# Performance work log

Measured on AMD Instinct MI355X. Metric: run time of the kernel, lower is better.

## Reference

```python
import jax, jax.numpy as jnp
import numpy as np

IMAGE_TOKEN_INDEX = -200
B, N, D = 2, 768, 2048          # batch, seq, llm_size
CLIP = 1024                      # clip hidden size
NUM_HEADS = 8
HEAD_DIM = CLIP // NUM_HEADS
NUM_LAYER, LAYER_RATE = 24, 4
LAYER_IDX = np.asarray(NUM_LAYER - np.arange(0, NUM_LAYER + 1, LAYER_RATE))  # [24,20,16,12,8,4,0]
J = len(LAYER_IDX)               # 7 selected layers
L = NUM_LAYER + 1                # 25 stacked layers in all_features
IMG, PATCH = 336, 14
HP = IMG // PATCH                # 24 patches per side; patch_ratio == 1
HW = HP * HP                     # 576 vision tokens
SL = HP * (HP + 1) + 1           # 601 = H*(W+1)+1 ragged slice length
SCALE = CLIP ** (-0.5)
LN_EPS = 1e-5
COS_EPS = 1e-8


def setup_inputs() -> dict:
    key = jax.random.key(0)
    ks = jax.random.split(key, 10)
    input_ids = jax.random.randint(ks[0], (B, N), 0, 32000)
    pos = jnp.array([37, 111])  # image-token positions; pos + SL <= N
    input_ids = input_ids.at[jnp.arange(B), pos].set(IMAGE_TOKEN_INDEX)
    rgb = jax.random.normal(ks[1], (B, 3, IMG, IMG), dtype=jnp.float32)
    mask = jnp.ones((B, 1, IMG, IMG), dtype=jnp.float32)  # last channel: all-ones mask
    images = jnp.concatenate([rgb, mask], axis=1)
    all_features = jax.random.normal(ks[2], (B, N, L, D), dtype=jnp.float32)
    patch_hw = jnp.full((B, 2), HP, dtype=jnp.int32)
    s = 0.02
    return {
        'input_ids': input_ids,
        'images': images,
        'all_features': all_features,
        'patch_hw': patch_hw,
        'norm_gamma': jnp.ones((J, D), dtype=jnp.float32),
        'norm_beta': jnp.zeros((J, D), dtype=jnp.float32),
        'norm_w': jax.random.normal(ks[3], (J, CLIP, D), dtype=jnp.float32) * s,
        'input_w': jax.random.normal(ks[4], (CLIP, D), dtype=jnp.float32) * s,
        'input_b': jnp.zeros((CLIP,), dtype=jnp.float32),
        'output_w': jax.random.normal(ks[5], (CLIP, CLIP), dtype=jnp.float32) * s,
        'output_b': jnp.zeros((CLIP,), dtype=jnp.float32),
        'clip_w': jax.random.normal(ks[6], (CLIP, 3 * PATCH * PATCH), dtype=jnp.float32) * s,
        'clip_b': jnp.zeros((CLIP,), dtype=jnp.float32),
    }


def reference(input_ids, images, all_features, patch_hw,
              norm_gamma, norm_beta, norm_w,
              input_w, input_b, output_w, output_b, clip_w, clip_b):
    # clip_layer modeled as a frozen 14x14 patch-embed linear -> [B, HW, CLIP]
    patches = images[:, :3].reshape(B, 3, HP, PATCH, HP, PATCH)
    patches = patches.transpose(0, 2, 4, 1, 3, 5).reshape(B, HW, 3 * PATCH * PATCH)
    clip_feats = patches @ clip_w.T + clip_b  # [B, HW, CLIP]
    # mask channel is all ones -> pooled clip_2d_mask keeps every patch
    lidx = jnp.asarray(LAYER_IDX)

    def per_sample(ids, feats, cf):
        # ragged slice at the image token (data-dependent start, fixed length)
        idx = jnp.argmax(ids == IMAGE_TOKEN_INDEX)
        f = jax.lax.dynamic_slice_in_dim(feats, idx, SL, axis=0)[1:]      # [600, L, D]
        # [L,D,H,W+1] drop-last-col in torch == row-major split here
        f = f.reshape(HP, HP + 1, L, D)[:, :HP].reshape(HW, L, D)          # [576, L, D]
        # per-layer LayerNorm + no-bias Linear on 7 selected layers
        xj = f[:, lidx]                                                    # [HW, J, D]
        mu = xj.mean(-1, keepdims=True)
        var = ((xj - mu) ** 2).mean(-1, keepdims=True)
        xn = (xj - mu) / jnp.sqrt(var + LN_EPS) * norm_gamma + norm_beta
        vis = jnp.einsum('njd,jcd->njc', xn, norm_w)                       # [HW, J, CLIP]
        inp = f[:, -1] @ input_w.T + input_b                               # [HW, CLIP]
        # single-query multi-head cross attention over the J-1 kv layers
        q = vis[:, 0].reshape(HW, NUM_HEADS, HEAD_DIM)                     # [HW, h, d]
        kv = vis[:, 1:].reshape(HW, J - 1, NUM_HEADS, HEAD_DIM).transpose(0, 2, 1, 3)  # [HW, h, J-1, d]
        attn = jax.nn.softmax((q[:, :, None, :] * SCALE * kv).sum(-1), axis=-1)        # [HW, h, J-1]
        fuse = (attn[..., None] * kv).sum(-2).reshape(HW, CLIP)
        out = inp + fuse @ output_w.T + output_b                           # [HW, CLIP]
        denom = jnp.maximum(jnp.linalg.norm(out, axis=-1) * jnp.linalg.norm(cf, axis=-1), COS_EPS)
        cos = (out * cf).sum(-1) / denom
        return 1.0 - cos.mean()

    losses = jax.vmap(per_sample)(input_ids, all_features, clip_feats)
    return losses.mean()  # mse_loss / count_image with count_image == B
```

## Files before the change

### kernel.cpp

```cpp
#include <hip/hip_runtime.h>

#define HW_   576
#define BHW   1152
#define DD    2048
#define CLIPC 1024
#define NSEQ  768
#define LL    25
#define KPAD  640

#define ASCALE 8.0f
#define BSCALE 32.0f
#define INV_AB (1.0f/256.0f)

typedef __bf16 bf16x8 __attribute__((ext_vector_type(8)));
typedef float  f32x4  __attribute__((ext_vector_type(4)));
typedef int    i32x8  __attribute__((ext_vector_type(8)));
typedef unsigned short u16;
typedef unsigned char  u8;

__device__ __forceinline__ float bf2f(u16 u){
  union { unsigned int i; float f; } v; v.i = ((unsigned int)u) << 16; return v.f;
}
__device__ __forceinline__ u16 f2bf(float f){
  union { float f; unsigned int i; } v; v.f = f;
  unsigned int u = v.i;
  return (u16)((u + 0x7fffu + ((u >> 16) & 1u)) >> 16);
}
__device__ __forceinline__ unsigned int pk2bf(float a, float b){
  return ((unsigned int)f2bf(a)) | (((unsigned int)f2bf(b)) << 16);
}
__device__ __forceinline__ unsigned int pk4_fp8(float a, float b, float c, float d){
  int v = 0;
  v = __builtin_amdgcn_cvt_pk_fp8_f32(a, b, v, false);
  v = __builtin_amdgcn_cvt_pk_fp8_f32(c, d, v, true);
  return (unsigned int)v;
}

__device__ __forceinline__ void gld_lds16(const void* g, void* l){
  __builtin_amdgcn_global_load_lds((__attribute__((address_space(1))) void*)g,
                                   (__attribute__((address_space(3))) void*)l,
                                   16, 0, 0);
}

__global__ void prep_k(const float* __restrict__ norm_w, const float* __restrict__ input_w,
                       const float* __restrict__ output_w, const float* __restrict__ clip_w,
                       const float* __restrict__ images, const float* __restrict__ feats,
                       const int* __restrict__ ids,
                       const float* __restrict__ gamma, const float* __restrict__ beta,
                       u8* __restrict__ B8, u16* __restrict__ inpw, u16* __restrict__ outw,
                       u16* __restrict__ clipw, u16* __restrict__ patch,
                       u8* __restrict__ A8, u16* __restrict__ A7,
                       float* __restrict__ rowacc, unsigned int* __restrict__ done){
  const int blk = blockIdx.x, tid = threadIdx.x;
  if (blk < 7168){
    long idx = (long)blk*2048 + tid*8;
    float4 v0 = *(const float4*)(norm_w + idx);
    float4 v1 = *(const float4*)(norm_w + idx + 4);
    uint2 o;
    o.x = pk4_fp8(v0.x*BSCALE, v0.y*BSCALE, v0.z*BSCALE, v0.w*BSCALE);
    o.y = pk4_fp8(v1.x*BSCALE, v1.y*BSCALE, v1.z*BSCALE, v1.w*BSCALE);
    *(uint2*)(B8 + idx) = o;
    return;
  }
  if (blk < 8704){
    const bool isInp = (blk < 8192);
    long idx = (long)(blk - (isInp ? 7168 : 8192))*2048 + tid*8;
    const float* s = isInp ? (input_w + idx) : (output_w + idx);
    float4 v0 = *(const float4*)s;
    float4 v1 = *(const float4*)(s + 4);
    uint4 o = { pk2bf(v0.x,v0.y), pk2bf(v0.z,v0.w), pk2bf(v1.x,v1.y), pk2bf(v1.z,v1.w) };
    *(uint4*)((isInp ? inpw : outw) + idx) = o;
    return;
  }
  if (blk < 9728){
    const int c = blk - 8704;
    for (int k = tid; k < KPAD; k += 256)
      clipw[c*KPAD + k] = (k < 588) ? f2bf(clip_w[c*588 + k]) : (u16)0;
    if (blk == 8704){
      for (int i = tid; i < BHW*4; i += 256) rowacc[i] = 0.f;
      if (tid == 0) *done = 0u;
    }
    return;
  }
  if (blk < 10880){
    const int r = blk - 9728;
    const int b = r / HW_, n = r % HW_;
    const int hi = n / 24, wi = n % 24;
    for (int p = tid; p < KPAD; p += 256){
      float v = 0.f;
      if (p < 588){
        int c3 = p / 196, rem = p - c3*196;
        int ph = rem / 14, pw = rem - ph*14;
        v = images[(((long)b*4 + c3)*336 + hi*14 + ph)*336 + wi*14 + pw];
      }
      patch[(long)r*KPAD + p] = f2bf(v);
    }
    return;
  }
  const int q = blk - 10880;
  const int r = q >> 3, g = q & 7;
  const int b = r / HW_, n = r % HW_;
  const int hi = n / 24, wi = n % 24;
  __shared__ int ridx[4];
  __shared__ float rs[4], rq[4];
  {
    int best = 0x7fffffff;
    for (int i = tid; i < NSEQ; i += 256)
      if (ids[b*NSEQ + i] == -200 && i < best) best = i;
    for (int off = 32; off; off >>= 1){ int o = __shfl_xor(best, off); best = min(best, o); }
    if ((tid & 63) == 0) ridx[tid >> 6] = best;
    __syncthreads();
  }
  const int tok = min(min(ridx[0],ridx[1]),min(ridx[2],ridx[3])) + 1 + hi*25 + wi;
  const int layer = (g < 7) ? (24 - g*4) : 24;
  const float* src = feats + (((long)(b*NSEQ + tok))*LL + layer)*DD + tid*8;
  float4 a = *(const float4*)src;
  float4 c = *(const float4*)(src + 4);
  if (g == 7){
    uint4 o = { pk2bf(a.x,a.y), pk2bf(a.z,a.w), pk2bf(c.x,c.y), pk2bf(c.z,c.w) };
    *(uint4*)(A7 + (long)r*DD + tid*8) = o;
    return;
  }
  float s  = a.x+a.y+a.z+a.w + c.x+c.y+c.z+c.w;
  float qq = a.x*a.x+a.y*a.y+a.z*a.z+a.w*a.w + c.x*c.x+c.y*c.y+c.z*c.z+c.w*c.w;
  for (int off = 32; off; off >>= 1){ s += __shfl_xor(s, off); qq += __shfl_xor(qq, off); }
  const int wave = tid >> 6, lane = tid & 63;
  if (lane == 0){ rs[wave] = s; rq[wave] = qq; }
  __syncthreads();
  const float ts = rs[0]+rs[1]+rs[2]+rs[3];
  const float tq = rq[0]+rq[1]+rq[2]+rq[3];
  const float mu   = ts * (1.f/2048.f);
  const float var  = tq * (1.f/2048.f) - mu*mu;
  const float rstd = rsqrtf(var + 1e-5f);
  const float4 g0 = *(const float4*)(gamma + g*DD + tid*8);
  const float4 g1 = *(const float4*)(gamma + g*DD + tid*8 + 4);
  const float4 b0 = *(const float4*)(beta  + g*DD + tid*8);
  const float4 b1 = *(const float4*)(beta  + g*DD + tid*8 + 4);
  uint2 o;
  o.x = pk4_fp8(((a.x-mu)*rstd*g0.x + b0.x)*ASCALE, ((a.y-mu)*rstd*g0.y + b0.y)*ASCALE,
                ((a.z-mu)*rstd*g0.z + b0.z)*ASCALE, ((a.w-mu)*rstd*g0.w + b0.w)*ASCALE);
  o.y = pk4_fp8(((c.x-mu)*rstd*g1.x + b1.x)*ASCALE, ((c.y-mu)*rstd*g1.y + b1.y)*ASCALE,
                ((c.z-mu)*rstd*g1.z + b1.z)*ASCALE, ((c.w-mu)*rstd*g1.w + b1.w)*ASCALE);
  *(uint2*)(A8 + ((long)g*BHW + r)*DD + tid*8) = o;
}

__global__ __launch_bounds__(256, 3)
void gemm9_k(const u8* __restrict__ A8, const u8* __restrict__ B8,
             u16* __restrict__ C_all, const u16* __restrict__ A7,
             const u16* __restrict__ inpw, const u16* __restrict__ patch,
             const u16* __restrict__ clipw, float* __restrict__ cf,
             const float* __restrict__ input_b, const float* __restrict__ clip_b){
  __shared__ alignas(16) u8 smem[32768];
  const int z = blockIdx.z;
  const int bm = blockIdx.x*128, bn = blockIdx.y*128;
  const int tid = threadIdx.x, wave = tid >> 6, lane = tid & 63;
  const int l15 = lane & 15, quad = lane >> 4;
  const int wr = (wave >> 1)*64, wc = (wave & 1)*64;
  f32x4 acc[4][4] = {};
  const int laneRow   = lane >> 3;
  const int laneChunk = (lane & 7) ^ laneRow;

  if (z < 7){
    u8* As = smem;
    u8* Bs = smem + 16384;
    const u8* Az = A8 + (long)z*BHW*DD;
    const u8* Bz = B8 + (long)z*CLIPC*DD;
    const u8* gA = Az + (long)(bm + wave*32 + laneRow)*DD + laneChunk*16;
    const u8* gB = Bz + (long)(bn + wave*32 + laneRow)*DD + laneChunk*16;
    u8* lA = &As[wave*32*128];
    u8* lB = &Bs[wave*32*128];
    const long rs8 = 8L*DD;
    for (int k0 = 0; k0 < DD; k0 += 128){
#pragma unroll
      for (int t = 0; t < 4; t++) gld_lds16(gA + k0 + t*rs8, lA + t*1024);
#pragma unroll
      for (int t = 0; t < 4; t++) gld_lds16(gB + k0 + t*rs8, lB + t*1024);
      __syncthreads();
      i32x8 af[4], bg[4];
      const int sw = l15 & 7;
#pragma unroll
      for (int i = 0; i < 4; i++){
        const u8* rp = &As[(wr + i*16 + l15)*128];
        uint4 lo = *(const uint4*)(rp + (((quad*2 + 0) ^ sw)*16));
        uint4 hi = *(const uint4*)(rp + (((quad*2 + 1) ^ sw)*16));
        af[i] = (i32x8){(int)lo.x,(int)lo.y,(int)lo.z,(int)lo.w,
                        (int)hi.x,(int)hi.y,(int)hi.z,(int)hi.w};
      }
#pragma unroll
      for (int j = 0; j < 4; j++){
        const u8* rp = &Bs[(wc + j*16 + l15)*128];
        uint4 lo = *(const uint4*)(rp + (((quad*2 + 0) ^ sw)*16));
        uint4 hi = *(const uint4*)(rp + (((quad*2 + 1) ^ sw)*16));
        bg[j] = (i32x8){(int)lo.x,(int)lo.y,(int)lo.z,(int)lo.w,
                        (int)hi.x,(int)hi.y,(int)hi.z,(int)hi.w};
      }
#pragma unroll
      for (int i = 0; i < 4; i++)
#pragma unroll
        for (int j = 0; j < 4; j++)
          acc[i][j] = __builtin_amdgcn_mfma_scale_f32_16x16x128_f8f6f4(
              af[i], bg[j], acc[i][j], 0, 0, 0, 0x7F7F7F7F, 0, 0x7F7F7F7F);
      __syncthreads();
    }
    u16* C = C_all + (long)z*BHW*CLIPC;
#pragma unroll
    for (int i = 0; i < 4; i++)
#pragma unroll
      for (int j = 0; j < 4; j++)
#pragma unroll
        for (int rr = 0; rr < 4; rr++){
          const int row = bm + wr + i*16 + quad*4 + rr;
          const int col = bn + wc + j*16 + l15;
          C[(long)row*CLIPC + col] = f2bf(acc[i][j][rr] * INV_AB);
        }
  } else {
    u16* As = (u16*)smem;
    u16* Bs = (u16*)(smem + 16384);
    const u16* Az = (z == 7) ? A7   : patch;
    const u16* Bz = (z == 7) ? inpw : clipw;
    const int K  = (z == 7) ? DD : KPAD;
    const int laneCol = laneChunk * 8;
    const u16* gA = Az + (long)(bm + wave*32 + laneRow)*K + laneCol;
    const u16* gB = Bz + (long)(bn + wave*32 + laneRow)*K + laneCol;
    u16* lA = &As[wave*2048];
    u16* lB = &Bs[wave*2048];
    const long rs8 = (long)8 * K;
    for (int k0 = 0; k0 < K; k0 += 64){
#pragma unroll
      for (int t = 0; t < 4; t++) gld_lds16(gA + k0 + t*rs8, lA + t*512);
#pragma unroll
      for (int t = 0; t < 4; t++) gld_lds16(gB + k0 + t*rs8, lB + t*512);
      __syncthreads();
#pragma unroll
      for (int s = 0; s < 2; s++){
        bf16x8 af[4], bg[4];
#pragma unroll
        for (int i = 0; i < 4; i++)
          af[i] = *(const bf16x8*)&As[(wr + i*16 + l15)*64 + (((s*4 + quad) ^ (l15 & 7))*8)];
#pragma unroll
        for (int j = 0; j < 4; j++)
          bg[j] = *(const bf16x8*)&Bs[(wc + j*16 + l15)*64 + (((s*4 + quad) ^ (l15 & 7))*8)];
#pragma unroll
        for (int i = 0; i < 4; i++)
#pragma unroll
          for (int j = 0; j < 4; j++)
            acc[i][j] = __builtin_amdgcn_mfma_f32_16x16x32_bf16(af[i], bg[j], acc[i][j], 0, 0, 0);
      }
      __syncthreads();
    }
    if (z == 7){
      u16* C = C_all + 7L*BHW*CLIPC;
#pragma unroll
      for (int i = 0; i < 4; i++)
#pragma unroll
        for (int j = 0; j < 4; j++)
#pragma unroll
          for (int rr = 0; rr < 4; rr++){
            const int row = bm + wr + i*16 + quad*4 + rr;
            const int col = bn + wc + j*16 + l15;
            C[(long)row*CLIPC + col] = f2bf(acc[i][j][rr] + input_b[col]);
          }
    } else {
#pragma unroll
      for (int i = 0; i < 4; i++)
#pragma unroll
        for (int j = 0; j < 4; j++)
#pragma unroll
          for (int rr = 0; rr < 4; rr++){
            const int row = bm + wr + i*16 + quad*4 + rr;
            const int col = bn + wc + j*16 + l15;
            cf[(long)row*CLIPC + col] = acc[i][j][rr] + clip_b[col];
          }
    }
  }
}

__global__ void attn_k(const u16* __restrict__ C_all, u16* __restrict__ fuse){
  const int r = blockIdx.x;
  const int h = (blockIdx.y << 2) | (threadIdx.x >> 6);
  const int lane = threadIdx.x & 63;
  const long slot = (long)BHW * CLIPC;
  const long rb = (long)r * CLIPC;
  const int c0 = h*128 + lane, c1 = c0 + 64;
  const float q0 = bf2f(C_all[rb + c0]), q1 = bf2f(C_all[rb + c1]);
  float k0v[6], k1v[6], dt[6];
#pragma unroll
  for (int t = 0; t < 6; t++){
    const u16* base = C_all + (long)(t+1)*slot + rb;
    k0v[t] = bf2f(base[c0]); k1v[t] = bf2f(base[c1]);
    dt[t] = q0*k0v[t] + q1*k1v[t];
  }
#pragma unroll
  for (int t = 0; t < 6; t++)
    for (int off = 32; off; off >>= 1) dt[t] += __shfl_xor(dt[t], off);
  float l[6], e[6];
#pragma unroll
  for (int t = 0; t < 6; t++) l[t] = dt[t] * 0.03125f;
  float m = l[0];
#pragma unroll
  for (int t = 1; t < 6; t++) m = fmaxf(m, l[t]);
  float ssum = 0.f;
#pragma unroll
  for (int t = 0; t < 6; t++){ e[t] = __expf(l[t] - m); ssum += e[t]; }
  const float inv = 1.f / ssum;
  float f0 = 0.f, f1 = 0.f;
#pragma unroll
  for (int t = 0; t < 6; t++){ const float a = e[t]*inv; f0 += a*k0v[t]; f1 += a*k1v[t]; }
  fuse[rb + c0] = f2bf(f0);
  fuse[rb + c1] = f2bf(f1);
}

__global__ __launch_bounds__(256, 3)
void gemm_out_k(const u16* __restrict__ fuse, const u16* __restrict__ outw,
                const u16* __restrict__ inp, const float* __restrict__ output_b,
                const float* __restrict__ cf, float* __restrict__ rowacc,
                unsigned int* __restrict__ done, float* __restrict__ out){
  __shared__ alignas(16) u8 smem[32768];
  u16* As = (u16*)smem;
  u16* Bs = (u16*)(smem + 16384);
  const int bm = blockIdx.x*128, bn = blockIdx.y*128;
  const int tid = threadIdx.x, wave = tid >> 6, lane = tid & 63;
  const int l15 = lane & 15, quad = lane >> 4;
  const int wr = (wave >> 1)*64, wc = (wave & 1)*64;
  f32x4 acc[4][4] = {};
  {
    const int laneRow = lane >> 3;
    const int laneCol = (((lane & 7) ^ laneRow) * 8);
    const u16* gA = fuse + (long)(bm + wave*32 + laneRow)*CLIPC + laneCol;
    const u16* gB = outw + (long)(bn + wave*32 + laneRow)*CLIPC + laneCol;
    u16* lA = &As[wave*2048];
    u16* lB = &Bs[wave*2048];
    const long rs8 = 8L*CLIPC;
    for (int k0 = 0; k0 < CLIPC; k0 += 64){
#pragma unroll
      for (int t = 0; t < 4; t++) gld_lds16(gA + k0 + t*rs8, lA + t*512);
#pragma unroll
      for (int t = 0; t < 4; t++) gld_lds16(gB + k0 + t*rs8, lB + t*512);
      __syncthreads();
#pragma unroll
      for (int s = 0; s < 2; s++){
        bf16x8 af[4], bg[4];
#pragma unroll
        for (int i = 0; i < 4; i++)
          af[i] = *(const bf16x8*)&As[(wr + i*16 + l15)*64 + (((s*4 + quad) ^ (l15 & 7))*8)];
#pragma unroll
        for (int j = 0; j < 4; j++)
          bg[j] = *(const bf16x8*)&Bs[(wc + j*16 + l15)*64 + (((s*4 + quad) ^ (l15 & 7))*8)];
#pragma unroll
        for (int i = 0; i < 4; i++)
#pragma unroll
          for (int j = 0; j < 4; j++)
            acc[i][j] = __builtin_amdgcn_mfma_f32_16x16x32_bf16(af[i], bg[j], acc[i][j], 0, 0, 0);
      }
      __syncthreads();
    }
  }
#pragma unroll
  for (int i = 0; i < 4; i++)
#pragma unroll
    for (int rr = 0; rr < 4; rr++){
      const int row = bm + wr + i*16 + quad*4 + rr;
      float soc = 0.f, soo = 0.f, scc = 0.f;
#pragma unroll
      for (int j = 0; j < 4; j++){
        const int col = bn + wc + j*16 + l15;
        const long p = (long)row*CLIPC + col;
        const float o = acc[i][j][rr] + output_b[col] + bf2f(inp[p]);
        const float c = cf[p];
        soc += o*c; soo += o*o; scc += c*c;
      }
#pragma unroll
      for (int off = 1; off < 16; off <<= 1){
        soc += __shfl_xor(soc, off); soo += __shfl_xor(soo, off); scc += __shfl_xor(scc, off);
      }
      if (l15 == 0){
        atomicAdd(&rowacc[row*4 + 0], soc);
        atomicAdd(&rowacc[row*4 + 1], soo);
        atomicAdd(&rowacc[row*4 + 2], scc);
      }
    }
  __threadfence();
  __shared__ unsigned int amLast;
  if (tid == 0) amLast = (atomicAdd(done, 1u) == 71u) ? 1u : 0u;
  __syncthreads();
  if (!amLast) return;
  float s = 0.f;
  for (int r = tid; r < BHW; r += 256){
    const float soc = __hip_atomic_load(&rowacc[r*4+0], __ATOMIC_RELAXED, __HIP_MEMORY_SCOPE_AGENT);
    const float soo = __hip_atomic_load(&rowacc[r*4+1], __ATOMIC_RELAXED, __HIP_MEMORY_SCOPE_AGENT);
    const float scc = __hip_atomic_load(&rowacc[r*4+2], __ATOMIC_RELAXED, __HIP_MEMORY_SCOPE_AGENT);
    s += soc / fmaxf(sqrtf(soo*scc), 1e-8f);
  }
  for (int off = 32; off; off >>= 1) s += __shfl_xor(s, off);
  __shared__ float fr[4];
  if ((tid & 63) == 0) fr[tid >> 6] = s;
  __syncthreads();
  if (tid == 0) out[0] = 1.f - (fr[0]+fr[1]+fr[2]+fr[3]) * (1.f/(float)BHW);
}

extern "C" void kernel_launch(void* const* d_in, const int* in_sizes, int n_in,
                              void* d_out, int out_size, void* d_ws, size_t ws_size,
                              hipStream_t stream){
  const int*   input_ids = (const int*)  d_in[0];
  const float* images    = (const float*)d_in[1];
  const float* all_feats = (const float*)d_in[2];
  const float* norm_gamma = (const float*)d_in[4];
  const float* norm_beta  = (const float*)d_in[5];
  const float* norm_w     = (const float*)d_in[6];
  const float* input_w    = (const float*)d_in[7];
  const float* input_b    = (const float*)d_in[8];
  const float* output_w   = (const float*)d_in[9];
  const float* output_b   = (const float*)d_in[10];
  const float* clip_w     = (const float*)d_in[11];
  const float* clip_b     = (const float*)d_in[12];
  float* out = (float*)d_out;

  char* w = (char*)d_ws;
  unsigned int* done = (unsigned int*)w;
  size_t off = 256;
  u8*  A8    = (u8*) (w + off); off += 7L*BHW*DD;
  u16* A7    = (u16*)(w + off); off += (long)BHW*DD*2;
  u8*  B8    = (u8*) (w + off); off += 7L*CLIPC*DD;
  u16* inpw  = (u16*)(w + off); off += (long)CLIPC*DD*2;
  u16* outw  = (u16*)(w + off); off += (long)CLIPC*CLIPC*2;
  u16* clipw = (u16*)(w + off); off += (long)CLIPC*KPAD*2;
  u16* patch = (u16*)(w + off); off += (long)BHW*KPAD*2;
  u16* C_all = (u16*)(w + off); off += 8L*BHW*CLIPC*2;
  u16* fuse  = (u16*)(w + off); off += (long)BHW*CLIPC*2;
  float* cf     = (float*)(w + off); off += (long)BHW*CLIPC*4;
  float* rowacc = (float*)(w + off); off += (long)BHW*4*4;

  prep_k<<<20096, 256, 0, stream>>>(norm_w, input_w, output_w, clip_w, images, all_feats,
                                    input_ids, norm_gamma, norm_beta,
                                    B8, inpw, outw, clipw, patch, A8, A7, rowacc, done);
  gemm9_k<<<dim3(9, 8, 9), 256, 0, stream>>>(A8, B8, C_all, A7, inpw, patch, clipw, cf,
                                             input_b, clip_b);
  attn_k<<<dim3(1152, 2), 256, 0, stream>>>(C_all, fuse);
  gemm_out_k<<<dim3(9, 8), 256, 0, stream>>>(fuse, outw, C_all + 7L*BHW*CLIPC,
                                             output_b, cf, rowacc, done, out);
}
```

Before: 531.9 us.

## Interleave GEMM problem blocks in flat grid and double-buffer output GEMM loads

The batched GEMM kernel now runs on a flattened 1D grid. Its first 576 blocks interleave the eight big GEMMs (z = f & 7), and the patch/clip GEMM tiles come last, so blocks working on the same tile position but different layers run together and the cheap K=640 work fills the tail. Separately, the output GEMM double-buffers its LDS tiles (64 KB) and prefetches the next K-slice while computing the current one. That overlap costs occupancy, since launch bounds drop to 2 blocks per CU. The output GEMM has only 72 blocks, so the lower occupancy limit hardly matters there.

```diff
diff --git a/kernel.cpp b/kernel.cpp
--- a/kernel.cpp
+++ b/kernel.cpp
@@ -151,8 +151,10 @@
              const u16* __restrict__ clipw, float* __restrict__ cf,
              const float* __restrict__ input_b, const float* __restrict__ clip_b){
   __shared__ alignas(16) u8 smem[32768];
-  const int z = blockIdx.z;
-  const int bm = blockIdx.x*128, bn = blockIdx.y*128;
+  const int f = blockIdx.x;
+  int z, t;
+  if (f < 576){ z = f & 7; t = f >> 3; } else { z = 8; t = f - 576; }
+  const int bm = (t % 9)*128, bn = (t / 9)*128;
   const int tid = threadIdx.x, wave = tid >> 6, lane = tid & 63;
   const int l15 = lane & 15, quad = lane >> 4;
   const int wr = (wave >> 1)*64, wc = (wave & 1)*64;
@@ -172,9 +174,9 @@
     const long rs8 = 8L*DD;
     for (int k0 = 0; k0 < DD; k0 += 128){
 #pragma unroll
-      for (int t = 0; t < 4; t++) gld_lds16(gA + k0 + t*rs8, lA + t*1024);
-#pragma unroll
-      for (int t = 0; t < 4; t++) gld_lds16(gB + k0 + t*rs8, lB + t*1024);
+      for (int t2 = 0; t2 < 4; t2++) gld_lds16(gA + k0 + t2*rs8, lA + t2*1024);
+#pragma unroll
+      for (int t2 = 0; t2 < 4; t2++) gld_lds16(gB + k0 + t2*rs8, lB + t2*1024);
       __syncthreads();
       i32x8 af[4], bg[4];
       const int sw = l15 & 7;
@@ -227,9 +229,9 @@
     const long rs8 = (long)8 * K;
     for (int k0 = 0; k0 < K; k0 += 64){
 #pragma unroll
-      for (int t = 0; t < 4; t++) gld_lds16(gA + k0 + t*rs8, lA + t*512);
-#pragma unroll
-      for (int t = 0; t < 4; t++) gld_lds16(gB + k0 + t*rs8, lB + t*512);
+      for (int t2 = 0; t2 < 4; t2++) gld_lds16(gA + k0 + t2*rs8, lA + t2*512);
+#pragma unroll
+      for (int t2 = 0; t2 < 4; t2++) gld_lds16(gB + k0 + t2*rs8, lB + t2*512);
       __syncthreads();
 #pragma unroll
       for (int s = 0; s < 2; s++){
@@ -310,14 +312,12 @@
   fuse[rb + c1] = f2bf(f1);
 }
 
-__global__ __launch_bounds__(256, 3)
+__global__ __launch_bounds__(256, 2)
 void gemm_out_k(const u16* __restrict__ fuse, const u16* __restrict__ outw,
                 const u16* __restrict__ inp, const float* __restrict__ output_b,
                 const float* __restrict__ cf, float* __restrict__ rowacc,
                 unsigned int* __restrict__ done, float* __restrict__ out){
-  __shared__ alignas(16) u8 smem[32768];
-  u16* As = (u16*)smem;
-  u16* Bs = (u16*)(smem + 16384);
+  __shared__ alignas(16) u8 smem[65536];
   const int bm = blockIdx.x*128, bn = blockIdx.y*128;
   const int tid = threadIdx.x, wave = tid >> 6, lane = tid & 63;
   const int l15 = lane & 15, quad = lane >> 4;
@@ -328,15 +328,24 @@
     const int laneCol = (((lane & 7) ^ laneRow) * 8);
     const u16* gA = fuse + (long)(bm + wave*32 + laneRow)*CLIPC + laneCol;
     const u16* gB = outw + (long)(bn + wave*32 + laneRow)*CLIPC + laneCol;
-    u16* lA = &As[wave*2048];
-    u16* lB = &Bs[wave*2048];
     const long rs8 = 8L*CLIPC;
+#pragma unroll
+    for (int t = 0; t < 4; t++) gld_lds16(gA + t*rs8, (u16*)smem + wave*2048 + t*512);
+#pragma unroll
+    for (int t = 0; t < 4; t++) gld_lds16(gB + t*rs8, (u16*)(smem + 16384) + wave*2048 + t*512);
+    __syncthreads();
     for (int k0 = 0; k0 < CLIPC; k0 += 64){
-#pragma unroll
-      for (int t = 0; t < 4; t++) gld_lds16(gA + k0 + t*rs8, lA + t*512);
-#pragma unroll
-      for (int t = 0; t < 4; t++) gld_lds16(gB + k0 + t*rs8, lB + t*512);
-      __syncthreads();
+      const int cur = (k0 >> 6) & 1;
+      if (k0 + 64 < CLIPC){
+        u16* lA = (u16*)(smem + (cur^1)*32768)         + wave*2048;
+        u16* lB = (u16*)(smem + (cur^1)*32768 + 16384) + wave*2048;
+#pragma unroll
+        for (int t = 0; t < 4; t++) gld_lds16(gA + (k0+64) + t*rs8, lA + t*512);
+#pragma unroll
+        for (int t = 0; t < 4; t++) gld_lds16(gB + (k0+64) + t*rs8, lB + t*512);
+      }
+      const u16* As = (const u16*)(smem + cur*32768);
+      const u16* Bs = (const u16*)(smem + cur*32768 + 16384);
 #pragma unroll
       for (int s = 0; s < 2; s++){
         bf16x8 af[4], bg[4];
@@ -433,8 +442,8 @@
   prep_k<<<20096, 256, 0, stream>>>(norm_w, input_w, output_w, clip_w, images, all_feats,
                                     input_ids, norm_gamma, norm_beta,
                                     B8, inpw, outw, clipw, patch, A8, A7, rowacc, done);
-  gemm9_k<<<dim3(9, 8, 9), 256, 0, stream>>>(A8, B8, C_all, A7, inpw, patch, clipw, cf,
-                                             input_b, clip_b);
+  gemm9_k<<<648, 256, 0, stream>>>(A8, B8, C_all, A7, inpw, patch, clipw, cf,
+                                   input_b, clip_b);
   attn_k<<<dim3(1152, 2), 256, 0, stream>>>(C_all, fuse);
   gemm_out_k<<<dim3(9, 8), 256, 0, stream>>>(fuse, outw, C_all + 7L*BHW*CLIPC,
                                              output_b, cf, rowacc, done, out);
```

Result: faster. 511.8 us (-3.8%).
